# Optimization experiments

Hardware: AMD Instinct MI355X
Metric: run time of the kernel (lower is better)

The kernel has to match this reference:

```python
import jax, jax.numpy as jnp
import numpy as np

THETA = 1.0
DILATIONS = (1, 2, 3, 4)
EPS = 1e-6


def _scale_features(x, d):
    # x: [B, C, H, W]; one pyramid scale (dilation d)
    B, C, H, W = x.shape
    k = 3 + 2 * (d - 1)          # kernel size per original formula
    pad = d * d                   # pad so effective span d*(k-1)+1 = 2d^2+1 preserves HxW
    K = k * k
    patches = jax.lax.conv_general_dilated_patches(
        x, (k, k), (1, 1), [(pad, pad), (pad, pad)], rhs_dilation=(d, d)
    )  # [B, C*K, H, W], channel-major per input channel
    p = patches.reshape(B, C, K, H, W)

    mu = p.mean(axis=2, keepdims=True)
    diff = p - mu
    var_biased = (diff * diff).mean(axis=2)                 # E[(p-mu)^2]
    std = jnp.sqrt(var_biased * (K / (K - 1))) + EPS        # torch .std is unbiased (ddof=1)

    contrast = var_biased / (std * std)                     # mean(normed^2)
    energy = (p * p).mean(axis=2)
    entropy = -(p * jnp.log(p + EPS)).mean(axis=2)
    # NB: original precedence -> 1.0 / mean(1 + |p - mu|)
    homogeneity = 1.0 / ((1.0 + jnp.abs(diff)).mean(axis=2))

    feats = jnp.stack([contrast, energy, entropy, homogeneity], axis=2)  # [B, C, 4, H, W]
    # martingale transform: exp(theta*log(f+eps) - 0.5*theta^2)
    M = jnp.exp(THETA * jnp.log(feats + EPS) - 0.5 * THETA ** 2)
    return M.reshape(B, C * 4, H, W)  # cat over channels of per-channel feature stacks


def setup_inputs() -> dict:
    key = jax.random.key(0)
    x = jax.random.uniform(key, (2, 4, 256, 256), dtype=jnp.float32)
    return {"x": x}


def reference(x):
    return tuple(_scale_features(x, d) for d in DILATIONS)
```

## Files before the change

kernel.cpp:

```cpp
#include <hip/hip_runtime.h>
#include <cstddef>

#define EPS 1e-6f
constexpr float INV_SQRT_E = 0.6065306597126334f;

template <int D>
__device__ __forceinline__ void body(const float* __restrict__ x,
                                     float* __restrict__ out,
                                     char* smem, int bc, int H, int W)
{
    constexpr int PAD = D * D;
    constexpr int KS  = 2 * D + 1;
    constexpr int K   = KS * KS;
    constexpr int TW  = 64, TH = 16;
    constexpr int LW  = TW + 2 * PAD;
    constexpr int LH  = TH + 2 * PAD;
    constexpr float INVK = 1.0f / (float)K;
    constexpr float UNB  = (float)K / (float)(K - 1);

    float2* sv = (float2*)smem;
    float2* rs2 = (float2*)(smem + LH * LW * 8);
    float*  rs1 = (float*) (smem + LH * LW * 8 + LH * 64 * 8);

    const int w0 = blockIdx.x * TW;
    const int h0 = blockIdx.y * TH;
    const float* xp = x + (size_t)bc * H * W;

    const int tid = threadIdx.y * 64 + threadIdx.x;
    for (int idx = tid; idx < LH * LW; idx += 1024) {
        const int r  = idx / LW;
        const int cc = idx - r * LW;
        const int gh = h0 - PAD + r;
        const int gw = w0 - PAD + cc;
        float v = 0.0f;
        if (gh >= 0 && gh < H && gw >= 0 && gw < W) v = xp[gh * W + gw];
        sv[idx] = make_float2(v, v * __logf(v + EPS));
    }
    __syncthreads();

    const int tx = threadIdx.x;
    const int ty = threadIdx.y;

    float s = 0.0f, s2 = 0.0f, sl = 0.0f;
    float sad;

    if constexpr (K <= 9) {
        const float2* base = &sv[ty * LW + tx];
        float ta[K];
        #pragma unroll
        for (int mi = 0; mi < KS; ++mi)
            #pragma unroll
            for (int mj = 0; mj < KS; ++mj) {
                const float2 p = base[(mi * D) * LW + mj * D];
                ta[mi * KS + mj] = p.x;
                s  += p.x;
                s2  = fmaf(p.x, p.x, s2);
                sl += p.y;
            }
        const float mu = s * INVK;
        sad = 0.0f;
        #pragma unroll
        for (int i = 0; i < K; ++i) sad += fabsf(ta[i] - mu);
    } else {
        for (int e = tid; e < LH * 64; e += 1024) {
            const int r = e >> 6;
            const int c = e & 63;
            const float2* rp = &sv[r * LW + c];
            float hs = 0.0f, hs2 = 0.0f, hsl = 0.0f;
            #pragma unroll
            for (int mj = 0; mj < KS; ++mj) {
                const float2 p = rp[mj * D];
                hs  += p.x;
                hs2  = fmaf(p.x, p.x, hs2);
                hsl += p.y;
            }
            rs2[e] = make_float2(hs, hs2);
            rs1[e] = hsl;
        }
        __syncthreads();

        #pragma unroll
        for (int mi = 0; mi < KS; ++mi) {
            const int rr = (ty + mi * D) * 64 + tx;
            const float2 q = rs2[rr];
            s  += q.x;
            s2 += q.y;
            sl += rs1[rr];
        }
        const float mu = s * INVK;

        const float2* base = &sv[ty * LW + tx];
        sad = 0.0f;
        #pragma unroll
        for (int mi = 0; mi < KS; ++mi)
            #pragma unroll
            for (int mj = 0; mj < KS; ++mj)
                sad += fabsf(base[(mi * D) * LW + mj * D].x - mu);
    }

    const float mu       = s * INVK;
    const float energy   = s2 * INVK;
    const float var      = fmaxf(energy - mu * mu, 0.0f);
    const float sd       = sqrtf(var * UNB) + EPS;
    const float contrast = var / (sd * sd);
    const float entropy  = -sl * INVK;
    const float homog    = 1.0f / (1.0f + sad * INVK);

    const size_t fstride = (size_t)H * W;
    const size_t rowoff  = (size_t)(h0 + ty) * W;
    float* op = out + (size_t)bc * 4 * fstride + w0 + tx;
    __builtin_nontemporal_store((contrast + EPS) * INV_SQRT_E, &op[0 * fstride + rowoff]);
    __builtin_nontemporal_store((energy   + EPS) * INV_SQRT_E, &op[1 * fstride + rowoff]);
    __builtin_nontemporal_store((entropy  + EPS) * INV_SQRT_E, &op[2 * fstride + rowoff]);
    __builtin_nontemporal_store((homog    + EPS) * INV_SQRT_E, &op[3 * fstride + rowoff]);
}

__global__ __launch_bounds__(1024, 4) void tex_fused(
    const float* __restrict__ x, float* __restrict__ out, int H, int W)
{
    extern __shared__ char smem[];
    const int dz = blockIdx.z & 3;
    const int bc = blockIdx.z >> 2;
    const size_t per = (size_t)8 * 4 * H * W;
    switch (dz) {
        case 0: body<1>(x, out + 0 * per, smem, bc, H, W); break;
        case 1: body<2>(x, out + 1 * per, smem, bc, H, W); break;
        case 2: body<3>(x, out + 2 * per, smem, bc, H, W); break;
        default: body<4>(x, out + 3 * per, smem, bc, H, W); break;
    }
}

extern "C" void kernel_launch(void* const* d_in, const int* in_sizes, int n_in,
                              void* d_out, int out_size, void* d_ws, size_t ws_size,
                              hipStream_t stream) {
    const float* x = (const float*)d_in[0];
    float* out = (float*)d_out;

    const int H = 256, W = 256;
    const size_t smem_bytes = 36864 + 24576 + 12288;

    dim3 blk(64, 16, 1);
    dim3 grd(W / 64, H / 16, 8 * 4);
    tex_fused<<<grd, blk, smem_bytes, stream>>>(x, out, H, W);
}
```

Measured before the change: 85.67 us.

## Halve tile height, switch to column-first separable sums, schedule heavy dilations first

Reduces block size from 1024 to 512 threads (tile 64x8) to cut shared memory per block and raise occupancy. For larger kernels, partial sums are now computed vertically per column over the full padded width, then summed horizontally, which shrinks the intermediate buffer to TH rows. Block z-index ordering is changed so the most expensive dilation (D=4) blocks are dispatched first for better load balance. The smaller tile increases halo overhead relative to useful output.

```diff
diff --git a/kernel.cpp b/kernel.cpp
--- a/kernel.cpp
+++ b/kernel.cpp
@@ -12,22 +12,22 @@
     constexpr int PAD = D * D;
     constexpr int KS  = 2 * D + 1;
     constexpr int K   = KS * KS;
-    constexpr int TW  = 64, TH = 16;
+    constexpr int TW  = 64, TH = 8;
     constexpr int LW  = TW + 2 * PAD;
     constexpr int LH  = TH + 2 * PAD;
     constexpr float INVK = 1.0f / (float)K;
     constexpr float UNB  = (float)K / (float)(K - 1);
 
-    float2* sv = (float2*)smem;
-    float2* rs2 = (float2*)(smem + LH * LW * 8);
-    float*  rs1 = (float*) (smem + LH * LW * 8 + LH * 64 * 8);
+    float2* sv  = (float2*)smem;
+    float2* cs2 = (float2*)(smem + LH * LW * 8);
+    float*  cs1 = (float*) (smem + LH * LW * 8 + TH * LW * 8);
 
     const int w0 = blockIdx.x * TW;
     const int h0 = blockIdx.y * TH;
     const float* xp = x + (size_t)bc * H * W;
 
     const int tid = threadIdx.y * 64 + threadIdx.x;
-    for (int idx = tid; idx < LH * LW; idx += 1024) {
+    for (int idx = tid; idx < LH * LW; idx += 512) {
         const int r  = idx / LW;
         const int cc = idx - r * LW;
         const int gh = h0 - PAD + r;
@@ -62,30 +62,31 @@
         #pragma unroll
         for (int i = 0; i < K; ++i) sad += fabsf(ta[i] - mu);
     } else {
-        for (int e = tid; e < LH * 64; e += 1024) {
-            const int r = e >> 6;
-            const int c = e & 63;
-            const float2* rp = &sv[r * LW + c];
-            float hs = 0.0f, hs2 = 0.0f, hsl = 0.0f;
+        for (int e = tid; e < TH * LW; e += 512) {
+            const int r = e / LW;
+            const int c = e - r * LW;
+            const float2* cp = &sv[r * LW + c];
+            float vs = 0.0f, vs2 = 0.0f, vsl = 0.0f;
             #pragma unroll
-            for (int mj = 0; mj < KS; ++mj) {
-                const float2 p = rp[mj * D];
-                hs  += p.x;
-                hs2  = fmaf(p.x, p.x, hs2);
-                hsl += p.y;
+            for (int mi = 0; mi < KS; ++mi) {
+                const float2 p = cp[(mi * D) * LW];
+                vs  += p.x;
+                vs2  = fmaf(p.x, p.x, vs2);
+                vsl += p.y;
             }
-            rs2[e] = make_float2(hs, hs2);
-            rs1[e] = hsl;
+            cs2[e] = make_float2(vs, vs2);
+            cs1[e] = vsl;
         }
         __syncthreads();
 
+        const float2* q2 = &cs2[ty * LW + tx];
+        const float*  q1 = &cs1[ty * LW + tx];
         #pragma unroll
-        for (int mi = 0; mi < KS; ++mi) {
-            const int rr = (ty + mi * D) * 64 + tx;
-            const float2 q = rs2[rr];
+        for (int mj = 0; mj < KS; ++mj) {
+            const float2 q = q2[mj * D];
             s  += q.x;
             s2 += q.y;
-            sl += rs1[rr];
+            sl += q1[mj * D];
         }
         const float mu = s * INVK;
 
@@ -115,18 +116,18 @@
     __builtin_nontemporal_store((homog    + EPS) * INV_SQRT_E, &op[3 * fstride + rowoff]);
 }
 
-__global__ __launch_bounds__(1024, 4) void tex_fused(
+__global__ __launch_bounds__(512, 8) void tex_fused(
     const float* __restrict__ x, float* __restrict__ out, int H, int W)
 {
     extern __shared__ char smem[];
-    const int dz = blockIdx.z & 3;
-    const int bc = blockIdx.z >> 2;
+    const int dz = blockIdx.z >> 3;
+    const int bc = blockIdx.z & 7;
     const size_t per = (size_t)8 * 4 * H * W;
     switch (dz) {
-        case 0: body<1>(x, out + 0 * per, smem, bc, H, W); break;
-        case 1: body<2>(x, out + 1 * per, smem, bc, H, W); break;
-        case 2: body<3>(x, out + 2 * per, smem, bc, H, W); break;
-        default: body<4>(x, out + 3 * per, smem, bc, H, W); break;
+        case 0: body<4>(x, out + 3 * per, smem, bc, H, W); break;
+        case 1: body<3>(x, out + 2 * per, smem, bc, H, W); break;
+        case 2: body<2>(x, out + 1 * per, smem, bc, H, W); break;
+        default: body<1>(x, out + 0 * per, smem, bc, H, W); break;
     }
 }
 
@@ -137,9 +138,9 @@
     float* out = (float*)d_out;
 
     const int H = 256, W = 256;
-    const size_t smem_bytes = 36864 + 24576 + 12288;
+    const size_t smem_bytes = 39936;
 
-    dim3 blk(64, 16, 1);
-    dim3 grd(W / 64, H / 16, 8 * 4);
+    dim3 blk(64, 8, 1);
+    dim3 grd(W / 64, H / 8, 8 * 4);
     tex_fused<<<grd, blk, smem_bytes, stream>>>(x, out, H, W);
 }
```

New measurement: 79.67 us. 7.0% less time.
